# Optimization experiments

Hardware: AMD Instinct MI355X
Metric: run time of the kernel (lower is better)

Reference implementation:

```python
import jax, jax.numpy as jnp
import numpy as np

B, S, H, E = 64, 512, 1024, 10  # batch, encoder seq len, hidden, n_events
LSTM_IN = H + 1 + E  # context (H) + x (1) + sim_scores (E)


def setup_inputs() -> dict:
    key = jax.random.key(0)
    ks = jax.random.split(key, 20)
    s = 0.02
    return {
        "x": jax.random.normal(ks[0], (B, 1), jnp.float32),
        "h0": jax.random.normal(ks[1], (1, B, H), jnp.float32),
        "c0": jax.random.normal(ks[2], (1, B, H), jnp.float32),
        "encoder_output": jax.random.normal(ks[3], (B, S, H), jnp.float32),
        "W_enc": jax.random.normal(ks[4], (H, H), jnp.float32) * s,
        "W_dec": jax.random.normal(ks[5], (H, H), jnp.float32) * s,
        "w_val": jax.random.normal(ks[6], (H,), jnp.float32) * s,
        "W_gate": jax.random.normal(ks[7], (E, E), jnp.float32) * s,
        "events_mat": jax.random.normal(ks[8], (E, H), jnp.float32) * s,
        "W_ih": jax.random.normal(ks[9], (4 * H, LSTM_IN), jnp.float32) * s,
        "W_hh": jax.random.normal(ks[10], (4 * H, H), jnp.float32) * s,
        "b_ih": jax.random.normal(ks[11], (4 * H,), jnp.float32) * s,
        "b_hh": jax.random.normal(ks[12], (4 * H,), jnp.float32) * s,
        "ln_g": jnp.ones((H,), jnp.float32),
        "ln_b": jnp.zeros((H,), jnp.float32),
        "W_fin": jax.random.normal(ks[13], (1, H), jnp.float32) * s,
        "b_fin": jnp.zeros((1,), jnp.float32),
    }


def reference(x, h0, c0, encoder_output, W_enc, W_dec, w_val, W_gate,
              events_mat, W_ih, W_hh, b_ih, b_hh, ln_g, ln_b, W_fin, b_fin):
    h = h0[0]  # [B,H] (num_layers == 1)
    c = c0[0]
    # Bahdanau attention: v^T tanh(W_e enc + W_d h)
    proj = jnp.einsum('bsh,gh->bsg', encoder_output, W_enc) + (h @ W_dec.T)[:, None, :]
    attn_scores = jnp.tanh(proj) @ w_val  # [B,S]
    attn_weight = jax.nn.softmax(attn_scores, axis=1)
    context = jnp.einsum('bs,bsh->bh', attn_weight, encoder_output)  # [B,H]
    # event similarity + gate
    sim_scores = (context @ events_mat.T) @ W_gate.T  # [B,E]
    # single-step LSTM on concat(context, sim, x)
    xin = jnp.concatenate([context, sim_scores, x], axis=1)  # [B, H+E+1]
    gates = xin @ W_ih.T + b_ih + h @ W_hh.T + b_hh  # [B,4H]
    i, f, g, o = jnp.split(gates, 4, axis=1)  # torch gate order: i,f,g,o
    c_new = jax.nn.sigmoid(f) * c + jax.nn.sigmoid(i) * jnp.tanh(g)
    h_new = jax.nn.sigmoid(o) * jnp.tanh(c_new)  # [B,H]
    # LayerNorm(eps=1e-5)
    mu = jnp.mean(h_new, axis=-1, keepdims=True)
    var = jnp.mean(jnp.square(h_new - mu), axis=-1, keepdims=True)
    y = (h_new - mu) / jnp.sqrt(var + 1e-5) * ln_g + ln_b
    fin_output = y @ W_fin.T + b_fin  # [B,1]
    return fin_output, (h_new[None], c_new[None]), attn_weight, sim_scores
```

## Files before the change

kernel.cpp:

```cpp
#include <hip/hip_runtime.h>
#include <math.h>

#define Bn 64
#define Sn 512
#define Hn 1024
#define En 10
#define Mn (Bn*Sn)
#define KIN 1035
#define KP  2112

#define OUT_FIN 0
#define OUT_H   64
#define OUT_C   65600
#define OUT_AW  131136
#define OUT_SIM 163904

#define WS_ENCB  0
#define WS_WENCB 16777216
#define WS_WTS   17301504
#define WS_PART  17334272
#define WS_CTXP  17334272
#define WS_WDECB 17858560
#define WS_H0B   18382848
#define WS_DPART 18415616
#define WS_GPART 4325376
#define WS_XINB  6422528

typedef __attribute__((ext_vector_type(8))) short bf16x8;
typedef __attribute__((ext_vector_type(4))) float f32x4;

#define ASYNC_CP16(gptr, lptr) \
  __builtin_amdgcn_global_load_lds((const __attribute__((address_space(1))) void*)(gptr), \
                                   (__attribute__((address_space(3))) void*)(lptr), 16, 0, 0)

static __device__ __forceinline__ unsigned short f2bf(float f) {
    union { float f; unsigned int u; } v; v.f = f;
    unsigned int r = (v.u + 0x7fffu + ((v.u >> 16) & 1u)) >> 16;
    return (unsigned short)r;
}
static __device__ __forceinline__ float bf2f(unsigned short h) {
    union { unsigned int u; float f; } v; v.u = ((unsigned int)h) << 16;
    return v.f;
}
static __device__ __forceinline__ float fast_tanh(float x) {
    float cx = fminf(15.f, fmaxf(-15.f, x));
    float e = __expf(2.f * cx);
    return (e - 1.f) * __builtin_amdgcn_rcpf(e + 1.f);
}

__global__ __launch_bounds__(256) void k_cast(const float* __restrict__ enc,
                                              const float* __restrict__ Wenc,
                                              const float* __restrict__ Wdec,
                                              const float* __restrict__ h0,
                                              unsigned short* __restrict__ encB,
                                              unsigned short* __restrict__ wencB,
                                              unsigned short* __restrict__ wdecB,
                                              unsigned short* __restrict__ h0B) {
    int bid = blockIdx.x;
    const float* src; unsigned short* dst; size_t off;
    if (bid < 16384)      { src = enc;  dst = encB;  off = (size_t)bid * 2048; }
    else if (bid < 16896) { src = Wenc; dst = wencB; off = (size_t)(bid - 16384) * 2048; }
    else if (bid < 17408) { src = Wdec; dst = wdecB; off = (size_t)(bid - 16896) * 2048; }
    else                  { src = h0;   dst = h0B;   off = (size_t)(bid - 17408) * 2048; }
    off += (size_t)threadIdx.x * 8;
    float4 v0 = *(const float4*)(src + off);
    float4 v1 = *(const float4*)(src + off + 4);
    ushort4 a; a.x = f2bf(v0.x); a.y = f2bf(v0.y); a.z = f2bf(v0.z); a.w = f2bf(v0.w);
    ushort4 b; b.x = f2bf(v1.x); b.y = f2bf(v1.y); b.z = f2bf(v1.z); b.w = f2bf(v1.w);
    *(ushort4*)(dst + off)     = a;
    *(ushort4*)(dst + off + 4) = b;
}

__global__ __launch_bounds__(256) void k1_gemm(const unsigned short* __restrict__ h0B,
                                               const unsigned short* __restrict__ wdecB,
                                               float* __restrict__ dpart) {
    __shared__ short As[4096];
    __shared__ short Bs[8192];

    const int n0 = blockIdx.x * 128;
    const int sp = blockIdx.y;
    const int kbeg = sp * 128;
    const int tid  = threadIdx.x;
    const int wave = tid >> 6;
    const int lane = tid & 63;
    const int wr = wave >> 1;
    const int wc = wave & 1;
    const int q4 = lane >> 4;
    const int ml = lane & 15;

    f32x4 acc[2][4];
#pragma unroll
    for (int i = 0; i < 2; ++i)
#pragma unroll
        for (int j = 0; j < 4; ++j) acc[i][j] = (f32x4){0.f, 0.f, 0.f, 0.f};

    const unsigned short* bTile = wdecB + (size_t)n0 * 1024;

    for (int kk = 0; kk < 2; ++kk) {
        int k0 = kbeg + kk * 64;
        __syncthreads();
#pragma unroll
        for (int t = 0; t < 2; ++t) {
            int q = wave * 2 + t;
            ASYNC_CP16(h0B + (size_t)lane * 1024 + k0 + q * 8, &As[(q * 64) * 8]);
        }
#pragma unroll
        for (int t = 0; t < 4; ++t) {
            int cb = t * 4 + wave;
            int q  = cb >> 1;
            int mb = (cb & 1) << 6;
            ASYNC_CP16(bTile + (size_t)(mb + lane) * 1024 + k0 + q * 8,
                       &Bs[(q * 128 + mb) * 8]);
        }
        __syncthreads();
#pragma unroll
        for (int s = 0; s < 2; ++s) {
            bf16x8 af[2], bfr[4];
#pragma unroll
            for (int i = 0; i < 2; ++i)
                af[i] = *(const bf16x8*)&As[((((s << 2) + q4) * 64) + wr * 32 + (i << 4) + ml) * 8];
#pragma unroll
            for (int j = 0; j < 4; ++j)
                bfr[j] = *(const bf16x8*)&Bs[((((s << 2) + q4) * 128) + wc * 64 + (j << 4) + ml) * 8];
#pragma unroll
            for (int i = 0; i < 2; ++i)
#pragma unroll
                for (int j = 0; j < 4; ++j)
                    acc[i][j] = __builtin_amdgcn_mfma_f32_16x16x32_bf16(af[i], bfr[j], acc[i][j], 0, 0, 0);
        }
    }
#pragma unroll
    for (int i = 0; i < 2; ++i)
#pragma unroll
        for (int j = 0; j < 4; ++j)
#pragma unroll
            for (int r = 0; r < 4; ++r) {
                int m = wr * 32 + (i << 4) + q4 * 4 + r;
                int n = n0 + wc * 64 + (j << 4) + ml;
                dpart[((size_t)sp * 64 + m) * 1024 + n] = acc[i][j][r];
            }
}

__global__ __launch_bounds__(512, 4) void k2_scores(const unsigned short* __restrict__ encB,
                                                    const unsigned short* __restrict__ wencB,
                                                    const float* __restrict__ dpart,
                                                    const float* __restrict__ wval,
                                                    float* __restrict__ part) {
    __shared__ short As[8192];
    __shared__ short Bs[8192];

    const int bid = blockIdx.x;
    const int xcd = bid & 7;
    const int j   = bid >> 3;
    const int m0  = (xcd * 32 + (j >> 3)) * 128;
    const int nb  = j & 7;
    const int n0  = nb * 128;
    const int b   = m0 >> 9;
    const int tid  = threadIdx.x;
    const int wave = tid >> 6;
    const int lane = tid & 63;
    const int wr = wave >> 1;
    const int wc = wave & 1;
    const int q4 = lane >> 4;
    const int ml = lane & 15;

    f32x4 acc[2][4];
#pragma unroll
    for (int i = 0; i < 2; ++i)
#pragma unroll
        for (int j2 = 0; j2 < 4; ++j2) acc[i][j2] = (f32x4){0.f, 0.f, 0.f, 0.f};

    const unsigned short* aTile = encB  + (size_t)m0 * 1024;
    const unsigned short* bTile = wencB + (size_t)n0 * 1024;

    for (int k0 = 0; k0 < 1024; k0 += 64) {
        __syncthreads();
#pragma unroll
        for (int t = 0; t < 4; ++t) {
            int c = t * 8 + wave;
            if (c < 16) {
                int q  = c >> 1;
                int mb = (c & 1) << 6;
                ASYNC_CP16(aTile + (size_t)(mb + lane) * 1024 + k0 + q * 8,
                           &As[(q * 128 + mb) * 8]);
            } else {
                int c2 = c - 16;
                int q  = c2 >> 1;
                int mb = (c2 & 1) << 6;
                ASYNC_CP16(bTile + (size_t)(mb + lane) * 1024 + k0 + q * 8,
                           &Bs[(q * 128 + mb) * 8]);
            }
        }
        __syncthreads();
#pragma unroll
        for (int s = 0; s < 2; ++s) {
            bf16x8 af[2], bfr[4];
            int q = (s << 2) + q4;
#pragma unroll
            for (int i = 0; i < 2; ++i)
                af[i] = *(const bf16x8*)&As[((q * 128) + wr * 32 + (i << 4) + ml) * 8];
#pragma unroll
            for (int j2 = 0; j2 < 4; ++j2)
                bfr[j2] = *(const bf16x8*)&Bs[((q * 128) + wc * 64 + (j2 << 4) + ml) * 8];
#pragma unroll
            for (int i = 0; i < 2; ++i)
#pragma unroll
                for (int j2 = 0; j2 < 4; ++j2)
                    acc[i][j2] = __builtin_amdgcn_mfma_f32_16x16x32_bf16(af[i], bfr[j2], acc[i][j2], 0, 0, 0);
        }
    }

    float dpv[4], wvv[4];
#pragma unroll
    for (int j2 = 0; j2 < 4; ++j2) {
        int n = n0 + wc * 64 + (j2 << 4) + ml;
        float d = 0.f;
#pragma unroll
        for (int sp = 0; sp < 8; ++sp) d += dpart[((size_t)sp * 64 + b) * 1024 + n];
        dpv[j2] = d;
        wvv[j2] = wval[n];
    }
    __syncthreads();
    float* rsum = (float*)As;
#pragma unroll
    for (int i = 0; i < 2; ++i) {
#pragma unroll
        for (int r = 0; r < 4; ++r) {
            float p = 0.f;
#pragma unroll
            for (int j2 = 0; j2 < 4; ++j2) p += fast_tanh(acc[i][j2][r] + dpv[j2]) * wvv[j2];
            p += __shfl_xor(p, 1);
            p += __shfl_xor(p, 2);
            p += __shfl_xor(p, 4);
            p += __shfl_xor(p, 8);
            if (ml == 0) rsum[wc * 128 + wr * 32 + (i << 4) + q4 * 4 + r] = p;
        }
    }
    __syncthreads();
    if (tid < 128)
        part[(size_t)nb * Mn + m0 + tid] = rsum[tid] + rsum[128 + tid];
}

__device__ __forceinline__ float block_sum256(float v, float* red, int tid) {
#pragma unroll
    for (int off = 1; off < 64; off <<= 1) v += __shfl_xor(v, off);
    if ((tid & 63) == 0) red[tid >> 6] = v;
    __syncthreads();
    v = red[0] + red[1] + red[2] + red[3];
    __syncthreads();
    return v;
}

__global__ __launch_bounds__(256) void k3a_softmax(const float* __restrict__ part,
                                                   float* __restrict__ wts,
                                                   float* __restrict__ out) {
    int b = blockIdx.x;
    int tid = threadIdx.x;
    __shared__ float red[8];
    int s0 = tid, s1 = tid + 256;
    float v0 = 0.f, v1 = 0.f;
#pragma unroll
    for (int nb = 0; nb < 8; ++nb) {
        v0 += part[(size_t)nb * Mn + b * 512 + s0];
        v1 += part[(size_t)nb * Mn + b * 512 + s1];
    }
    float mx = fmaxf(v0, v1);
#pragma unroll
    for (int off = 1; off < 64; off <<= 1) mx = fmaxf(mx, __shfl_xor(mx, off));
    if ((tid & 63) == 0) red[tid >> 6] = mx;
    __syncthreads();
    mx = fmaxf(fmaxf(red[0], red[1]), fmaxf(red[2], red[3]));
    __syncthreads();
    float e0 = __expf(v0 - mx), e1 = __expf(v1 - mx);
    float sm = block_sum256(e0 + e1, red, tid);
    float inv = 1.0f / sm;
    float w0 = e0 * inv, w1 = e1 * inv;
    wts[b * 512 + s0] = w0;
    wts[b * 512 + s1] = w1;
    out[OUT_AW + b * 512 + s0] = w0;
    out[OUT_AW + b * 512 + s1] = w1;
}

__global__ __launch_bounds__(256) void k3b_context(const unsigned short* __restrict__ encB,
                                                   const float* __restrict__ wts,
                                                   float* __restrict__ ctxp) {
    int b  = blockIdx.y;
    int sc = blockIdx.x >> 1;
    int hh = blockIdx.x & 1;
    int tid = threadIdx.x;
    int sr = tid >> 7;
    int cl = tid & 127;
    int hc = hh * 512 + cl * 4;
    const unsigned short* e = encB + (size_t)b * Sn * Hn + (size_t)sc * 64 * Hn + hc;
    const float* w = wts + b * 512 + sc * 64;
    float a0 = 0.f, a1 = 0.f, a2 = 0.f, a3 = 0.f;
#pragma unroll 8
    for (int s = sr; s < 64; s += 2) {
        uint2 p = *(const uint2*)(e + (size_t)s * 1024);
        float ws = w[s];
        a0 += ws * bf2f((unsigned short)(p.x & 0xffffu));
        a1 += ws * bf2f((unsigned short)(p.x >> 16));
        a2 += ws * bf2f((unsigned short)(p.y & 0xffffu));
        a3 += ws * bf2f((unsigned short)(p.y >> 16));
    }
    __shared__ float lds[512];
    if (sr == 1) *(float4*)&lds[cl * 4] = (float4){a0, a1, a2, a3};
    __syncthreads();
    if (sr == 0) {
        float4 o = *(const float4*)&lds[cl * 4];
        o.x += a0; o.y += a1; o.z += a2; o.w += a3;
        *(float4*)(ctxp + ((size_t)sc * 64 + b) * 1024 + hc) = o;
    }
}

__global__ __launch_bounds__(256) void k4_sim(const float* __restrict__ ctxp,
                                              const float* __restrict__ events,
                                              const float* __restrict__ Wg,
                                              const float* __restrict__ x,
                                              const float* __restrict__ h0,
                                              float* __restrict__ out,
                                              unsigned short* __restrict__ xinB) {
    int b = blockIdx.x;
    int tid = threadIdx.x, wv = tid >> 6, lane = tid & 63;
    __shared__ float cl[1024];
    __shared__ float tmp[16];
    unsigned short* xrow = xinB + (size_t)b * KP;
#pragma unroll
    for (int i = 0; i < 4; ++i) {
        int h = tid + i * 256;
        float v = 0.f;
#pragma unroll
        for (int sc = 0; sc < 8; ++sc) v += ctxp[((size_t)sc * 64 + b) * 1024 + h];
        cl[h] = v;
        xrow[h] = f2bf(v);
        xrow[1035 + h] = f2bf(h0[b * 1024 + h]);
    }
    if (tid == 0) xrow[1034] = f2bf(x[b]);
    if (tid < 53) xrow[2059 + tid] = 0;
    __syncthreads();
    for (int e = wv; e < 10; e += 4) {
        const float* ev = events + e * 1024;
        float a = 0.f;
#pragma unroll
        for (int kk = 0; kk < 1024; kk += 64) a += cl[kk + lane] * ev[kk + lane];
#pragma unroll
        for (int off = 1; off < 64; off <<= 1) a += __shfl_xor(a, off);
        if (lane == 0) tmp[e] = a;
    }
    __syncthreads();
    if (tid < 10) {
        float s2 = 0.f;
#pragma unroll
        for (int e = 0; e < 10; ++e) s2 += Wg[tid * 10 + e] * tmp[e];
        out[OUT_SIM + b * 10 + tid] = s2;
        xrow[1024 + tid] = f2bf(s2);
    }
}

__global__ __launch_bounds__(256) void k5_gemm(const unsigned short* __restrict__ xinB,
                                               const float* __restrict__ Wih,
                                               const float* __restrict__ Whh,
                                               float* __restrict__ gpart) {
    __shared__ short As[4096];
    __shared__ short Bs[8192];

    const int n0 = blockIdx.x * 128;
    const int sp = blockIdx.y;
    const int kbeg   = (sp == 0) ? 0 : (5 + (sp - 1) * 4) * 64;
    const int ksteps = (sp == 0) ? 5 : 4;
    const int tid  = threadIdx.x;
    const int wave = tid >> 6;
    const int lane = tid & 63;
    const int wr = wave >> 1;
    const int wc = wave & 1;
    const int q4 = lane >> 4;
    const int ml = lane & 15;

    f32x4 acc[2][4];
#pragma unroll
    for (int i = 0; i < 2; ++i)
#pragma unroll
        for (int j = 0; j < 4; ++j) acc[i][j] = (f32x4){0.f, 0.f, 0.f, 0.f};

    for (int kk = 0; kk < ksteps; ++kk) {
        int k0 = kbeg + kk * 64;
        __syncthreads();
#pragma unroll
        for (int t = 0; t < 2; ++t) {
            int q = wave * 2 + t;
            ASYNC_CP16(xinB + (size_t)lane * KP + k0 + q * 8, &As[(q * 64) * 8]);
        }
#pragma unroll
        for (int t = 0; t < 4; ++t) {
            int cb = t * 4 + wave;
            int q  = cb >> 1;
            int mb = (cb & 1) << 6;
            int g  = n0 + mb + lane;
            int kq = k0 + q * 8;
            const float* rih = Wih + (size_t)g * 1035;
            const float* rhh = Whh + (size_t)g * 1024 - 1035;
            union { unsigned short us[8]; bf16x8 v; } pk;
#pragma unroll
            for (int e2 = 0; e2 < 8; ++e2) {
                int k = kq + e2;
                float vv;
                if (k < 1035)      vv = rih[k];
                else if (k < 2059) vv = rhh[k];
                else               vv = 0.f;
                pk.us[e2] = f2bf(vv);
            }
            *(bf16x8*)&Bs[(q * 128 + mb + lane) * 8] = pk.v;
        }
        __syncthreads();
#pragma unroll
        for (int s = 0; s < 2; ++s) {
            bf16x8 af[2], bfr[4];
#pragma unroll
            for (int i = 0; i < 2; ++i)
                af[i] = *(const bf16x8*)&As[((((s << 2) + q4) * 64) + wr * 32 + (i << 4) + ml) * 8];
#pragma unroll
            for (int j = 0; j < 4; ++j)
                bfr[j] = *(const bf16x8*)&Bs[((((s << 2) + q4) * 128) + wc * 64 + (j << 4) + ml) * 8];
#pragma unroll
            for (int i = 0; i < 2; ++i)
#pragma unroll
                for (int j = 0; j < 4; ++j)
                    acc[i][j] = __builtin_amdgcn_mfma_f32_16x16x32_bf16(af[i], bfr[j], acc[i][j], 0, 0, 0);
        }
    }
#pragma unroll
    for (int i = 0; i < 2; ++i)
#pragma unroll
        for (int j = 0; j < 4; ++j)
#pragma unroll
            for (int r = 0; r < 4; ++r) {
                int m = wr * 32 + (i << 4) + q4 * 4 + r;
                int n = n0 + wc * 64 + (j << 4) + ml;
                gpart[((size_t)sp * 64 + m) * 4096 + n] = acc[i][j][r];
            }
}

__global__ __launch_bounds__(256) void k56_lstm_ln(const float* __restrict__ gpart,
                                                   const float* __restrict__ bih,
                                                   const float* __restrict__ bhh,
                                                   const float* __restrict__ c0,
                                                   const float* __restrict__ lng,
                                                   const float* __restrict__ lnb,
                                                   const float* __restrict__ Wfin,
                                                   const float* __restrict__ bfin,
                                                   float* __restrict__ out) {
    int b = blockIdx.x, tid = threadIdx.x;
    __shared__ float red[8];
    float hn[4];
#pragma unroll
    for (int r = 0; r < 4; ++r) {
        int u = tid + (r << 8);
        float g[4];
#pragma unroll
        for (int gt = 0; gt < 4; ++gt) {
            int rr = gt * 1024 + u;
            float a = bih[rr] + bhh[rr];
#pragma unroll
            for (int sp = 0; sp < 8; ++sp)
                a += gpart[((size_t)sp * 64 + b) * 4096 + rr];
            g[gt] = a;
        }
        float cp = c0[b * 1024 + u];
        float si = 1.f / (1.f + __expf(-g[0]));
        float sf = 1.f / (1.f + __expf(-g[1]));
        float so = 1.f / (1.f + __expf(-g[3]));
        float cn = sf * cp + si * tanhf(g[2]);
        hn[r] = so * tanhf(cn);
        out[OUT_H + b * 1024 + u] = hn[r];
        out[OUT_C + b * 1024 + u] = cn;
    }
    float mu = block_sum256(hn[0] + hn[1] + hn[2] + hn[3], red, tid) * (1.f / 1024.f);
    float d0 = hn[0] - mu, d1 = hn[1] - mu, d2 = hn[2] - mu, d3 = hn[3] - mu;
    float var = block_sum256(d0 * d0 + d1 * d1 + d2 * d2 + d3 * d3, red, tid) * (1.f / 1024.f);
    float rstd = rsqrtf(var + 1e-5f);
    float acc = (d0 * rstd * lng[tid]       + lnb[tid])       * Wfin[tid]
              + (d1 * rstd * lng[tid + 256] + lnb[tid + 256]) * Wfin[tid + 256]
              + (d2 * rstd * lng[tid + 512] + lnb[tid + 512]) * Wfin[tid + 512]
              + (d3 * rstd * lng[tid + 768] + lnb[tid + 768]) * Wfin[tid + 768];
    acc = block_sum256(acc, red, tid);
    if (tid == 0) out[OUT_FIN + b] = acc + bfin[0];
}

extern "C" void kernel_launch(void* const* d_in, const int* in_sizes, int n_in,
                              void* d_out, int out_size, void* d_ws, size_t ws_size,
                              hipStream_t stream) {
    (void)in_sizes; (void)n_in; (void)out_size; (void)ws_size;
    const float* x    = (const float*)d_in[0];
    const float* h0   = (const float*)d_in[1];
    const float* c0   = (const float*)d_in[2];
    const float* enc  = (const float*)d_in[3];
    const float* Wenc = (const float*)d_in[4];
    const float* Wdec = (const float*)d_in[5];
    const float* wval = (const float*)d_in[6];
    const float* Wg   = (const float*)d_in[7];
    const float* ev   = (const float*)d_in[8];
    const float* Wih  = (const float*)d_in[9];
    const float* Whh  = (const float*)d_in[10];
    const float* bih  = (const float*)d_in[11];
    const float* bhh  = (const float*)d_in[12];
    const float* lng  = (const float*)d_in[13];
    const float* lnb  = (const float*)d_in[14];
    const float* Wfin = (const float*)d_in[15];
    const float* bfin = (const float*)d_in[16];

    float* out  = (float*)d_out;
    float* ws   = (float*)d_ws;
    unsigned short* encB  = (unsigned short*)(ws + WS_ENCB);
    unsigned short* wencB = (unsigned short*)(ws + WS_WENCB);
    unsigned short* wdecB = (unsigned short*)(ws + WS_WDECB);
    unsigned short* h0B   = (unsigned short*)(ws + WS_H0B);
    float* dpart = ws + WS_DPART;
    float* wts   = ws + WS_WTS;
    float* part  = ws + WS_PART;
    float* ctxp  = ws + WS_CTXP;
    float* gpart = ws + WS_GPART;
    unsigned short* xinB  = (unsigned short*)(ws + WS_XINB);

    k_cast     <<<17440, 256, 0, stream>>>(enc, Wenc, Wdec, h0, encB, wencB, wdecB, h0B);
    k1_gemm    <<<dim3(8, 8), 256, 0, stream>>>(h0B, wdecB, dpart);
    k2_scores  <<<2048, 512, 0, stream>>>(encB, wencB, dpart, wval, part);
    k3a_softmax<<<64, 256, 0, stream>>>(part, wts, out);
    k3b_context<<<dim3(16, 64), 256, 0, stream>>>(encB, wts, ctxp);
    k4_sim     <<<64, 256, 0, stream>>>(ctxp, ev, Wg, x, h0, out, xinB);
    k5_gemm    <<<dim3(32, 8), 256, 0, stream>>>(xinB, Wih, Whh, gpart);
    k56_lstm_ln<<<64, 256, 0, stream>>>(gpart, bih, bhh, c0, lng, lnb, Wfin, bfin, out);
}
```

Before: 452.4 us.

## Enlarge score GEMM tiles to 256x256 with double-buffered LDS staging

The attention score GEMM tile grows from 128x128 to 256x256, with each wave computing a 128x64 sub-tile, and the grid shrinks from 2048 blocks to 512. LDS staging becomes double-buffered so the async copies for the next K-slice overlap with the MFMA work on the current one. The softmax kernel now sums 4 column partials instead of 8. The aim is to raise arithmetic intensity, cut global/LDS traffic and partial-sum writes, and hide load latency, at the cost of 128 accumulator registers per thread, 128 KB of LDS, lower occupancy and fewer blocks relative to the CU count.

```diff
diff --git a/kernel.cpp b/kernel.cpp
--- a/kernel.cpp
+++ b/kernel.cpp
@@ -141,104 +141,110 @@
             }
 }
 
-__global__ __launch_bounds__(512, 4) void k2_scores(const unsigned short* __restrict__ encB,
-                                                    const unsigned short* __restrict__ wencB,
-                                                    const float* __restrict__ dpart,
-                                                    const float* __restrict__ wval,
-                                                    float* __restrict__ part) {
-    __shared__ short As[8192];
-    __shared__ short Bs[8192];
+__global__ __launch_bounds__(512) void k2_scores(const unsigned short* __restrict__ encB,
+                                                 const unsigned short* __restrict__ wencB,
+                                                 const float* __restrict__ dpart,
+                                                 const float* __restrict__ wval,
+                                                 float* __restrict__ part) {
+    __shared__ short As[2][16384];
+    __shared__ short Bs[2][16384];
 
     const int bid = blockIdx.x;
     const int xcd = bid & 7;
     const int j   = bid >> 3;
-    const int m0  = (xcd * 32 + (j >> 3)) * 128;
-    const int nb  = j & 7;
-    const int n0  = nb * 128;
+    const int m0  = (xcd * 16 + (j >> 2)) * 256;
+    const int nb  = j & 3;
+    const int n0  = nb * 256;
     const int b   = m0 >> 9;
     const int tid  = threadIdx.x;
     const int wave = tid >> 6;
     const int lane = tid & 63;
-    const int wr = wave >> 1;
-    const int wc = wave & 1;
+    const int wr2 = wave >> 2;
+    const int wc2 = wave & 3;
     const int q4 = lane >> 4;
     const int ml = lane & 15;
 
-    f32x4 acc[2][4];
-#pragma unroll
-    for (int i = 0; i < 2; ++i)
-#pragma unroll
-        for (int j2 = 0; j2 < 4; ++j2) acc[i][j2] = (f32x4){0.f, 0.f, 0.f, 0.f};
+    f32x4 acc[8][4];
+#pragma unroll
+    for (int i = 0; i < 8; ++i)
+#pragma unroll
+        for (int jj = 0; jj < 4; ++jj) acc[i][jj] = (f32x4){0.f, 0.f, 0.f, 0.f};
 
     const unsigned short* aTile = encB  + (size_t)m0 * 1024;
     const unsigned short* bTile = wencB + (size_t)n0 * 1024;
 
-    for (int k0 = 0; k0 < 1024; k0 += 64) {
+    auto STAGE = [&](int kt, int bf) {
+        int k0 = kt * 64;
+#pragma unroll
+        for (int t2 = 0; t2 < 4; ++t2) {
+            int c  = t2 * 8 + wave;
+            int q  = c >> 2;
+            int sg = (c & 3) * 64;
+            ASYNC_CP16(aTile + (size_t)(sg + lane) * 1024 + k0 + q * 8,
+                       &As[bf][(q * 256 + sg) * 8]);
+            ASYNC_CP16(bTile + (size_t)(sg + lane) * 1024 + k0 + q * 8,
+                       &Bs[bf][(q * 256 + sg) * 8]);
+        }
+    };
+
+    STAGE(0, 0);
+    __syncthreads();
+
+    for (int t = 0; t < 16; ++t) {
+        const int cur = t & 1;
+        if (t < 15) STAGE(t + 1, cur ^ 1);
+        bf16x8 bfr[2][4];
+#pragma unroll
+        for (int s = 0; s < 2; ++s)
+#pragma unroll
+            for (int jj = 0; jj < 4; ++jj)
+                bfr[s][jj] = *(const bf16x8*)
+                    &Bs[cur][(((s * 4 + q4) * 256) + wc2 * 64 + jj * 16 + ml) * 8];
+#pragma unroll
+        for (int i = 0; i < 8; ++i) {
+            bf16x8 a0 = *(const bf16x8*)
+                &As[cur][((q4 * 256) + wr2 * 128 + i * 16 + ml) * 8];
+            bf16x8 a1 = *(const bf16x8*)
+                &As[cur][(((4 + q4) * 256) + wr2 * 128 + i * 16 + ml) * 8];
+#pragma unroll
+            for (int jj = 0; jj < 4; ++jj)
+                acc[i][jj] = __builtin_amdgcn_mfma_f32_16x16x32_bf16(a0, bfr[0][jj], acc[i][jj], 0, 0, 0);
+#pragma unroll
+            for (int jj = 0; jj < 4; ++jj)
+                acc[i][jj] = __builtin_amdgcn_mfma_f32_16x16x32_bf16(a1, bfr[1][jj], acc[i][jj], 0, 0, 0);
+        }
         __syncthreads();
-#pragma unroll
-        for (int t = 0; t < 4; ++t) {
-            int c = t * 8 + wave;
-            if (c < 16) {
-                int q  = c >> 1;
-                int mb = (c & 1) << 6;
-                ASYNC_CP16(aTile + (size_t)(mb + lane) * 1024 + k0 + q * 8,
-                           &As[(q * 128 + mb) * 8]);
-            } else {
-                int c2 = c - 16;
-                int q  = c2 >> 1;
-                int mb = (c2 & 1) << 6;
-                ASYNC_CP16(bTile + (size_t)(mb + lane) * 1024 + k0 + q * 8,
-                           &Bs[(q * 128 + mb) * 8]);
-            }
-        }
-        __syncthreads();
-#pragma unroll
-        for (int s = 0; s < 2; ++s) {
-            bf16x8 af[2], bfr[4];
-            int q = (s << 2) + q4;
-#pragma unroll
-            for (int i = 0; i < 2; ++i)
-                af[i] = *(const bf16x8*)&As[((q * 128) + wr * 32 + (i << 4) + ml) * 8];
-#pragma unroll
-            for (int j2 = 0; j2 < 4; ++j2)
-                bfr[j2] = *(const bf16x8*)&Bs[((q * 128) + wc * 64 + (j2 << 4) + ml) * 8];
-#pragma unroll
-            for (int i = 0; i < 2; ++i)
-#pragma unroll
-                for (int j2 = 0; j2 < 4; ++j2)
-                    acc[i][j2] = __builtin_amdgcn_mfma_f32_16x16x32_bf16(af[i], bfr[j2], acc[i][j2], 0, 0, 0);
-        }
     }
 
     float dpv[4], wvv[4];
 #pragma unroll
-    for (int j2 = 0; j2 < 4; ++j2) {
-        int n = n0 + wc * 64 + (j2 << 4) + ml;
+    for (int jj = 0; jj < 4; ++jj) {
+        int n = n0 + wc2 * 64 + jj * 16 + ml;
         float d = 0.f;
 #pragma unroll
         for (int sp = 0; sp < 8; ++sp) d += dpart[((size_t)sp * 64 + b) * 1024 + n];
-        dpv[j2] = d;
-        wvv[j2] = wval[n];
-    }
-    __syncthreads();
+        dpv[jj] = d;
+        wvv[jj] = wval[n];
+    }
     float* rsum = (float*)As;
 #pragma unroll
-    for (int i = 0; i < 2; ++i) {
+    for (int i = 0; i < 8; ++i) {
 #pragma unroll
         for (int r = 0; r < 4; ++r) {
             float p = 0.f;
 #pragma unroll
-            for (int j2 = 0; j2 < 4; ++j2) p += fast_tanh(acc[i][j2][r] + dpv[j2]) * wvv[j2];
+            for (int jj = 0; jj < 4; ++jj) p += fast_tanh(acc[i][jj][r] + dpv[jj]) * wvv[jj];
             p += __shfl_xor(p, 1);
             p += __shfl_xor(p, 2);
             p += __shfl_xor(p, 4);
             p += __shfl_xor(p, 8);
-            if (ml == 0) rsum[wc * 128 + wr * 32 + (i << 4) + q4 * 4 + r] = p;
-        }
-    }
-    __syncthreads();
-    if (tid < 128)
-        part[(size_t)nb * Mn + m0 + tid] = rsum[tid] + rsum[128 + tid];
+            if (ml == 0) rsum[wc2 * 256 + wr2 * 128 + i * 16 + q4 * 4 + r] = p;
+        }
+    }
+    __syncthreads();
+    if (tid < 256)
+        part[(size_t)nb * Mn + m0 + tid] =
+            rsum[tid] + rsum[256 + tid] + rsum[512 + tid] + rsum[768 + tid];
 }
 
 __device__ __forceinline__ float block_sum256(float v, float* red, int tid) {
@@ -260,7 +266,7 @@
     int s0 = tid, s1 = tid + 256;
     float v0 = 0.f, v1 = 0.f;
 #pragma unroll
-    for (int nb = 0; nb < 8; ++nb) {
+    for (int nb = 0; nb < 4; ++nb) {
         v0 += part[(size_t)nb * Mn + b * 512 + s0];
         v1 += part[(size_t)nb * Mn + b * 512 + s1];
     }
@@ -523,7 +529,7 @@
 
     k_cast     <<<17440, 256, 0, stream>>>(enc, Wenc, Wdec, h0, encB, wencB, wdecB, h0B);
     k1_gemm    <<<dim3(8, 8), 256, 0, stream>>>(h0B, wdecB, dpart);
-    k2_scores  <<<2048, 512, 0, stream>>>(encB, wencB, dpart, wval, part);
+    k2_scores  <<<512, 512, 0, stream>>>(encB, wencB, dpart, wval, part);
     k3a_softmax<<<64, 256, 0, stream>>>(part, wts, out);
     k3b_context<<<dim3(16, 64), 256, 0, stream>>>(encB, wts, ctxp);
     k4_sim     <<<64, 256, 0, stream>>>(ctxp, ev, Wg, x, h0, out, xinB);
```

Measured after the change: 478.3 us. +5.7%, slower.
